# Performance work log

Measured on AMD Instinct MI355X. Metric: run time of the kernel, lower is better.

## Reference

```python
import jax, jax.numpy as jnp
import numpy as np
import math

B, S, E, H = 2, 8192, 1024, 16
D = E // H  # 64
CHUNK = 128


def _build_slopes(n):
    # ALiBi-style slopes (n is a power of 2 here)
    start = 2.0 ** (-(2.0 ** -(math.log2(n) - 3)))
    return np.array([start * (start ** i) for i in range(n)], dtype=np.float32)


def setup_inputs() -> dict:
    key = jax.random.key(0)
    ks = jax.random.split(key, 6)
    x = jax.random.normal(ks[0], (B, S, E), dtype=jnp.float32)
    # rotary table: (S, D//2, 2) = (cos, sin)
    inv_freq = 1.0 / (10000.0 ** (np.arange(0, D, 2, dtype=np.float32) / D))
    ang = np.arange(S, dtype=np.float32)[:, None] * inv_freq[None, :]  # (S, D/2)
    freqs_cis = jnp.asarray(np.stack([np.cos(ang), np.sin(ang)], axis=-1))
    wq = jax.random.normal(ks[1], (E, E), dtype=jnp.float32) * 0.02
    wk = jax.random.normal(ks[2], (E, E), dtype=jnp.float32) * 0.02
    wv = jax.random.normal(ks[3], (E, E), dtype=jnp.float32) * 0.02
    wo = jax.random.normal(ks[4], (E, E), dtype=jnp.float32) * 0.02
    rms_w = jnp.ones((E,), dtype=jnp.float32)
    return {"x": x, "freqs_cis": freqs_cis, "wq": wq, "wk": wk, "wv": wv, "wo": wo, "rms_w": rms_w}


def apply_rotary(x, fc):
    # x: (b, s, h, d); fc: (s, d/2, 2)
    xr = x.reshape(*x.shape[:-1], -1, 2)          # (b,s,h,d/2,2)
    fc = fc[None, :, None, :, :]                   # (1,s,1,d/2,2)
    out = jnp.stack([
        xr[..., 0] * fc[..., 0] - xr[..., 1] * fc[..., 1],
        xr[..., 1] * fc[..., 0] + xr[..., 0] * fc[..., 1],
    ], axis=-1)
    return out.reshape(x.shape)


def lightning_attn(q, k, v, slopes, C=CHUNK):
    # q,k,v: (B,H,S,D); per-head decay lambda = exp(-slope)
    Bs, Hs, Ss, Ds = q.shape
    NC = Ss // C
    j = jnp.arange(C, dtype=jnp.float32)
    diff = j[:, None] - j[None, :]
    s3 = slopes[:, None, None]                     # (H,1,1)
    Dmask = jnp.where(diff >= 0, jnp.exp(-s3 * diff), 0.0)   # (H,C,C) intra decay
    q_dec = jnp.exp(-slopes[:, None] * (j + 1.0))             # (H,C) cross-chunk q decay
    k_dec = jnp.exp(-slopes[:, None] * (C - 1.0 - j))         # (H,C) state-update k decay
    c_dec = jnp.exp(-slopes * C)[None, :, None, None]         # (1,H,1,1) full-chunk decay
    qc = q.reshape(Bs, Hs, NC, C, Ds).transpose(2, 0, 1, 3, 4)
    kc = k.reshape(Bs, Hs, NC, C, Ds).transpose(2, 0, 1, 3, 4)
    vc = v.reshape(Bs, Hs, NC, C, Ds).transpose(2, 0, 1, 3, 4)

    def step(St, inp):
        qb, kb, vb = inp                                       # (B,H,C,D)
        scores = jnp.einsum('bhid,bhjd->bhij', qb, kb) * Dmask[None]
        o = jnp.einsum('bhij,bhjd->bhid', scores, vb)
        o = o + q_dec[None, :, :, None] * jnp.einsum('bhid,bhde->bhie', qb, St)
        St = c_dec * St + jnp.einsum('bhcd,bhce->bhde', kb * k_dec[None, :, :, None], vb)
        return St, o

    S0 = jnp.zeros((Bs, Hs, Ds, Ds), dtype=jnp.float32)
    _, oc = jax.lax.scan(step, S0, (qc, kc, vc))               # oc: (NC,B,H,C,D)
    return oc.transpose(1, 2, 0, 3, 4).reshape(Bs, Hs, Ss, Ds)


def rms_norm(x, w, eps=1e-5):
    xf = x.astype(jnp.float32)
    n = xf * jax.lax.rsqrt(jnp.mean(xf * xf, axis=-1, keepdims=True) + eps)
    return n.astype(x.dtype) * w


def reference(x, freqs_cis, wq, wk, wv, wo, rms_w):
    b, s, _ = x.shape
    slopes = jnp.asarray(_build_slopes(H))
    q = (x @ wq.T).reshape(b, s, H, D)
    k = (x @ wk.T).reshape(b, s, H, D)
    v = (x @ wv.T).reshape(b, s, H, D)
    q = apply_rotary(q, freqs_cis)
    k = apply_rotary(k, freqs_cis)
    q = q.transpose(0, 2, 1, 3)   # (B,H,S,D)
    k = k.transpose(0, 2, 1, 3)
    v = v.transpose(0, 2, 1, 3)
    o = lightning_attn(q, k, v, slopes)             # (B,H,S,D)
    o = o.transpose(0, 2, 1, 3).reshape(b, s, E)    # b n (h d)
    o = rms_norm(o, rms_w)
    return o @ wo.T
```

## Files before the change

### kernel.cpp

```cpp
#include <hip/hip_runtime.h>


using h16   = _Float16;
using h16x8 = __attribute__((ext_vector_type(8))) _Float16;
using h16x4 = __attribute__((ext_vector_type(4))) _Float16;
using f32x4 = __attribute__((ext_vector_type(4))) float;

#define MFMA16(a,b,c) __builtin_amdgcn_mfma_f32_16x16x32_f16(a,b,c,0,0,0)

#define GLOAD16(gp, lp) __builtin_amdgcn_global_load_lds( \
    (const __attribute__((address_space(1))) void*)(gp),  \
    (__attribute__((address_space(3))) void*)(lp), 16, 0, 0)

__device__ __forceinline__ h16x8 rope8(h16x8 v, const float* __restrict__ fp) {
  float4 f0 = *(const float4*)fp;
  float4 f1 = *(const float4*)(fp + 4);
  h16x8 o; float x0, x1;
  x0=(float)v[0]; x1=(float)v[1]; o[0]=(h16)(x0*f0.x - x1*f0.y); o[1]=(h16)(x1*f0.x + x0*f0.y);
  x0=(float)v[2]; x1=(float)v[3]; o[2]=(h16)(x0*f0.z - x1*f0.w); o[3]=(h16)(x1*f0.z + x0*f0.w);
  x0=(float)v[4]; x1=(float)v[5]; o[4]=(h16)(x0*f1.x - x1*f1.y); o[5]=(h16)(x1*f1.x + x0*f1.y);
  x0=(float)v[6]; x1=(float)v[7]; o[6]=(h16)(x0*f1.z - x1*f1.w); o[7]=(h16)(x1*f1.z + x0*f1.w);
  return o;
}

__global__ __launch_bounds__(256) void k_cvt(const float* __restrict__ s,
                                             h16* __restrict__ d, int n) {
  int i = (blockIdx.x * 256 + threadIdx.x) * 8;
  if (i >= n) return;
  float4 a = *(const float4*)(s + i);
  float4 b = *(const float4*)(s + i + 4);
  h16x8 o;
  o[0]=(h16)a.x; o[1]=(h16)a.y; o[2]=(h16)a.z; o[3]=(h16)a.w;
  o[4]=(h16)b.x; o[5]=(h16)b.y; o[6]=(h16)b.z; o[7]=(h16)b.w;
  *(h16x8*)(d + i) = o;
}

__global__ __launch_bounds__(256) void k_cvt4(
    const float* __restrict__ s0, const float* __restrict__ s1,
    const float* __restrict__ s2, const float* __restrict__ s3,
    h16* __restrict__ d0, h16* __restrict__ d1,
    h16* __restrict__ d2, h16* __restrict__ d3) {
  const float* s = blockIdx.y == 0 ? s0 : (blockIdx.y == 1 ? s1 : (blockIdx.y == 2 ? s2 : s3));
  h16* d        = blockIdx.y == 0 ? d0 : (blockIdx.y == 1 ? d1 : (blockIdx.y == 2 ? d2 : d3));
  int i = (blockIdx.x * 256 + threadIdx.x) * 8;
  float4 a = *(const float4*)(s + i);
  float4 b = *(const float4*)(s + i + 4);
  h16x8 o;
  o[0]=(h16)a.x; o[1]=(h16)a.y; o[2]=(h16)a.z; o[3]=(h16)a.w;
  o[4]=(h16)b.x; o[5]=(h16)b.y; o[6]=(h16)b.z; o[7]=(h16)b.w;
  *(h16x8*)(d + i) = o;
}

__device__ __forceinline__ void gemm256_loop(
    const h16* __restrict__ At, const h16* __restrict__ Bt,
    char* smem, int w, int l, f32x4 (&acc)[8][4])
{
  const int tid = w*64 + l;
  const int wr = w >> 2, wc = w & 3;

  size_t gof[2];
  #pragma unroll
  for (int c = 0; c < 2; c++) {
    int G = c*512 + tid;
    int pp = G >> 3;
    int idx = (G & 7) ^ (pp & 7);
    gof[c] = (size_t)(2*pp + (idx >> 2))*1024 + (idx & 3)*8;
  }

  const int q16 = ((((l & 1) << 2) | (l >> 4)) ^ ((l >> 1) & 7)) * 16;
  const int abyte = wr*8192 + ((l >> 1) & 7)*128 + q16;
  const int bbyte = 16384 + wc*4096 + ((l >> 1) & 7)*128 + q16;

  auto stageA = [&](int kt) {
    char* buf = smem + (kt & 3)*32768;
    #pragma unroll
    for (int c = 0; c < 2; c++)
      GLOAD16(At + gof[c] + kt*32, buf + c*8192 + w*1024);
  };
  auto stageB = [&](int kt) {
    char* buf = smem + (kt & 3)*32768;
    #pragma unroll
    for (int c = 0; c < 2; c++)
      GLOAD16(Bt + gof[c] + kt*32, buf + 16384 + c*8192 + w*1024);
  };

  stageA(0); stageB(0); stageA(1); stageB(1);
  asm volatile("s_waitcnt vmcnt(4)" ::: "memory");
  __builtin_amdgcn_sched_barrier(0);
  __builtin_amdgcn_s_barrier();

  for (int t = 0; t < 32; ++t) {
    const char* buf = smem + (t & 3)*32768;
    h16x8 af[8], bf[4];
    #pragma unroll
    for (int mf = 0; mf < 4; mf++) af[mf] = *(const h16x8*)(buf + abyte + mf*1024);
    #pragma unroll
    for (int nf = 0; nf < 4; nf++) bf[nf] = *(const h16x8*)(buf + bbyte + nf*1024);
    if (t < 30) stageA(t + 2);
    asm volatile("s_waitcnt lgkmcnt(0)" ::: "memory");
    __builtin_amdgcn_sched_barrier(0);
    __builtin_amdgcn_s_setprio(1);
    #pragma unroll
    for (int mf = 0; mf < 4; mf++)
      #pragma unroll
      for (int nf = 0; nf < 4; nf++)
        acc[mf][nf] = MFMA16(af[mf], bf[nf], acc[mf][nf]);
    __builtin_amdgcn_s_setprio(0);
    #pragma unroll
    for (int mf = 0; mf < 4; mf++) af[4+mf] = *(const h16x8*)(buf + abyte + 4096 + mf*1024);
    if (t < 30) stageB(t + 2);
    asm volatile("s_waitcnt lgkmcnt(0)" ::: "memory");
    __builtin_amdgcn_sched_barrier(0);
    __builtin_amdgcn_s_setprio(1);
    #pragma unroll
    for (int mf = 0; mf < 4; mf++)
      #pragma unroll
      for (int nf = 0; nf < 4; nf++)
        acc[4+mf][nf] = MFMA16(af[4+mf], bf[nf], acc[4+mf][nf]);
    __builtin_amdgcn_s_setprio(0);
    if (t < 30)       asm volatile("s_waitcnt vmcnt(4)" ::: "memory");
    else if (t == 30) asm volatile("s_waitcnt vmcnt(0)" ::: "memory");
    if (t < 31) {
      __builtin_amdgcn_sched_barrier(0);
      __builtin_amdgcn_s_barrier();
    }
  }
}

__global__ __launch_bounds__(512, 2) void k_qkv(
    const h16* __restrict__ xh, const h16* __restrict__ w3,
    h16* __restrict__ qn, h16* __restrict__ kn, h16* __restrict__ vn)
{
  extern __shared__ __align__(16) char smem[];
  const int tid = threadIdx.x;
  const int w = tid >> 6, l = tid & 63;
  const int m0 = blockIdx.x * 256;
  const int nt = blockIdx.y;
  const int wr = w >> 2, wc = w & 3;

  f32x4 acc[8][4] = {};
  gemm256_loop(xh + (size_t)m0*1024, w3 + (size_t)(nt*256)*1024, smem, w, l, acc);

  const int proj = nt >> 2;
  h16* dst = proj == 0 ? qn : (proj == 1 ? kn : vn);
  const int cb = (nt & 3)*256 + wc*64;
  #pragma unroll
  for (int mf = 0; mf < 8; mf++)
    #pragma unroll
    for (int nf = 0; nf < 4; nf++)
      #pragma unroll
      for (int r = 0; r < 4; r++) {
        int row = wr*128 + mf*16 + ((l >> 4) << 2) + r;
        int col = cb + nf*16 + (l & 15);
        dst[(size_t)(m0 + row)*1024 + col] = (h16)acc[mf][nf][r];
      }
}

__global__ __launch_bounds__(512, 2) void k_out(
    const h16* __restrict__ an, const h16* __restrict__ woh,
    float* __restrict__ out)
{
  extern __shared__ __align__(16) char smem[];
  const int tid = threadIdx.x;
  const int w = tid >> 6, l = tid & 63;
  const int m0 = blockIdx.x * 256;
  const int n0 = blockIdx.y * 256;
  const int wr = w >> 2, wc = w & 3;

  f32x4 acc[8][4] = {};
  gemm256_loop(an + (size_t)m0*1024, woh + (size_t)n0*1024, smem, w, l, acc);

  #pragma unroll
  for (int mf = 0; mf < 8; mf++)
    #pragma unroll
    for (int nf = 0; nf < 4; nf++)
      #pragma unroll
      for (int r = 0; r < 4; r++) {
        int row = wr*128 + mf*16 + ((l >> 4) << 2) + r;
        int col = n0 + wc*64 + nf*16 + (l & 15);
        out[(size_t)(m0 + row)*1024 + col] = acc[mf][nf][r];
      }
}

__global__ __launch_bounds__(256) void k_trkv(
    const h16* __restrict__ kn, const h16* __restrict__ vn,
    const float* __restrict__ fc,
    h16* __restrict__ vt, h16* __restrict__ Th)
{
  __shared__ __align__(16) h16 tl[128*64];
  __shared__ __align__(16) h16 kT2[64*136];
  __shared__ __align__(16) h16 vT2[64*136];
  __shared__ float dt[128];
  const int tid = threadIdx.x;
  const int st = blockIdx.x;
  const int bh = blockIdx.y;
  const int b = bh >> 4, h = bh & 15;
  if (tid < 128) {
    float slope = exp2f(-0.5f * (float)(h + 1));
    dt[tid] = expf(-slope * (float)(127 - tid));
  }
  const size_t ibase = ((size_t)(b*8192 + st*128))*1024 + h*64;
  const size_t obase = (size_t)bh*64*8192 + st*128;
  const int cr = tid >> 3, c8 = tid & 7;

  for (int which = 0; which < 2; ++which) {
    const h16* src = which ? vn : kn;
    h16* dT2 = which ? vT2 : kT2;
    __syncthreads();
    #pragma unroll
    for (int i = 0; i < 4; i++) {
      int r = i*32 + cr;
      h16x8 v = *(const h16x8*)(src + ibase + (size_t)r*1024 + c8*8);
      if (!which) v = rope8(v, fc + (size_t)(st*128 + r)*64 + c8*8);
      int slot = (c8 + ((r >> 3) & 7)) & 7;
      *(h16x8*)(tl + r*64 + slot*8) = v;
    }
    __syncthreads();
    #pragma unroll
    for (int i = 0; i < 4; i++) {
      int chunk = i*256 + tid;
      int d = chunk >> 4;
      int j8 = chunk & 15;
      h16x8 o;
      #pragma unroll
      for (int jj = 0; jj < 8; jj++) {
        int c = j8*8 + jj;
        int pos = (d + ((c >> 3) & 7)*8) & 63;
        float fv = (float)tl[c*64 + pos];
        if (!which) fv *= dt[c];
        o[jj] = (h16)fv;
      }
      *(h16x8*)(dT2 + d*136 + j8*8) = o;
      if (which) *(h16x8*)(vt + obase + (size_t)d*8192 + j8*8) = o;
    }
  }
  __syncthreads();

  const int w = tid >> 6, l = tid & 63;
  f32x4 acc[4] = {};
  h16x8 a[4];
  #pragma unroll
  for (int ks = 0; ks < 4; ks++)
    a[ks] = *(const h16x8*)(vT2 + (w*16 + (l & 15))*136 + ks*32 + (l >> 4)*8);
  #pragma unroll
  for (int nf = 0; nf < 4; nf++) {
    #pragma unroll
    for (int ks = 0; ks < 4; ks++) {
      h16x8 bfr = *(const h16x8*)(kT2 + (nf*16 + (l & 15))*136 + ks*32 + (l >> 4)*8);
      acc[nf] = MFMA16(a[ks], bfr, acc[nf]);
    }
  }
  h16* Tb = Th + ((size_t)bh*64 + st)*4096;
  #pragma unroll
  for (int nf = 0; nf < 4; nf++)
    #pragma unroll
    for (int r = 0; r < 4; r++) {
      int e = w*16 + ((l >> 4) << 2) + r;
      int d = nf*16 + (l & 15);
      Tb[e*64 + d] = (h16)acc[nf][r];
    }
}

__global__ __launch_bounds__(256) void k_scan(const h16* __restrict__ Th,
                                              h16* __restrict__ ph) {
  const int bh = blockIdx.x;
  const int j  = blockIdx.y * 256 + threadIdx.x;
  const int h = bh & 15;
  const float cdec = expf(-exp2f(-0.5f*(float)(h+1)) * 128.0f);
  const h16* Tb = Th + (size_t)bh*64*4096 + j;
  h16* pb = ph + (size_t)bh*64*4096 + j;
  float run = 0.f;
  for (int t = 0; t < 64; t++) {
    float kv = (float)Tb[(size_t)t*4096];
    pb[(size_t)t*4096] = (h16)run;
    run = cdec*run + kv;
  }
}

__global__ __launch_bounds__(256) void k_att(
    const h16* __restrict__ qn, const h16* __restrict__ kn,
    const float* __restrict__ fc,
    const h16* __restrict__ vt, const h16* __restrict__ ph,
    h16* __restrict__ oh)
{
  __shared__ __align__(16) h16 P[128*144];
  __shared__ float dt[128], qd[128];
  const int tid = threadIdx.x;
  const int t = blockIdx.x;
  const int bh = blockIdx.y;
  const int b = bh >> 4, h = bh & 15;
  if (tid < 128) {
    float slope = exp2f(-0.5f*(float)(h+1));
    dt[tid] = expf(-slope*(float)tid);
    qd[tid] = expf(-slope*(float)(tid+1));
  }
  __syncthreads();
  const int w = tid >> 6, l = tid & 63;
  const int iw = w * 32;
  const h16* qb = qn + ((size_t)(b*8192 + t*128))*1024 + h*64;
  const h16* kb = kn + ((size_t)(b*8192 + t*128))*1024 + h*64;
  const h16* vb = vt + (size_t)bh*64*8192 + t*128;
  const h16* pb = ph + ((size_t)bh*64 + t)*4096;
  const float* fcb = fc + (size_t)(t*128)*64;

  h16x8 aq[2][2];
  #pragma unroll
  for (int mf = 0; mf < 2; mf++)
    #pragma unroll
    for (int ks = 0; ks < 2; ks++) {
      int row = iw + mf*16 + (l & 15);
      int d0 = ks*32 + (l >> 4)*8;
      aq[mf][ks] = rope8(*(const h16x8*)(qb + (size_t)row*1024 + d0),
                         fcb + (size_t)row*64 + d0);
    }

  f32x4 sc[2][8] = {};
  #pragma unroll
  for (int nf = 0; nf < 8; nf++) {
    if (nf*16 <= iw + 31) {
      #pragma unroll
      for (int ks = 0; ks < 2; ks++) {
        int row = nf*16 + (l & 15);
        int d0 = ks*32 + (l >> 4)*8;
        h16x8 bk = rope8(*(const h16x8*)(kb + (size_t)row*1024 + d0),
                         fcb + (size_t)row*64 + d0);
        sc[0][nf] = MFMA16(aq[0][ks], bk, sc[0][nf]);
        sc[1][nf] = MFMA16(aq[1][ks], bk, sc[1][nf]);
      }
    }
  }
  #pragma unroll
  for (int mf = 0; mf < 2; mf++) {
    #pragma unroll
    for (int nf = 0; nf < 8; nf++) {
      #pragma unroll
      for (int r = 0; r < 4; r++) {
        int i = iw + mf*16 + ((l >> 4) << 2) + r;
        int j = nf*16 + (l & 15);
        int diff = i - j;
        float v = diff >= 0 ? sc[mf][nf][r]*dt[diff] : 0.f;
        P[i*144 + j] = (h16)v;
      }
    }
  }
  f32x4 ao[2][4] = {};
  #pragma unroll
  for (int kc = 0; kc < 4; kc++) {
    h16x8 ap0 = *(const h16x8*)(P + (size_t)(iw + (l & 15))*144 + kc*32 + (l >> 4)*8);
    h16x8 ap1 = *(const h16x8*)(P + (size_t)(iw + 16 + (l & 15))*144 + kc*32 + (l >> 4)*8);
    #pragma unroll
    for (int nf = 0; nf < 4; nf++) {
      h16x8 bv = *(const h16x8*)(vb + (size_t)(nf*16 + (l & 15))*8192 + kc*32 + (l >> 4)*8);
      ao[0][nf] = MFMA16(ap0, bv, ao[0][nf]);
      ao[1][nf] = MFMA16(ap1, bv, ao[1][nf]);
    }
  }
  f32x4 a2[2][4] = {};
  #pragma unroll
  for (int ks = 0; ks < 2; ks++) {
    #pragma unroll
    for (int nf = 0; nf < 4; nf++) {
      h16x8 bs = *(const h16x8*)(pb + (size_t)(nf*16 + (l & 15))*64 + ks*32 + (l >> 4)*8);
      a2[0][nf] = MFMA16(aq[0][ks], bs, a2[0][nf]);
      a2[1][nf] = MFMA16(aq[1][ks], bs, a2[1][nf]);
    }
  }
  #pragma unroll
  for (int mf = 0; mf < 2; mf++) {
    #pragma unroll
    for (int nf = 0; nf < 4; nf++) {
      #pragma unroll
      for (int r = 0; r < 4; r++) {
        int i = iw + mf*16 + ((l >> 4) << 2) + r;
        int e = nf*16 + (l & 15);
        float o = ao[mf][nf][r] + qd[i]*a2[mf][nf][r];
        int s = t*128 + i;
        oh[((size_t)(b*8192 + s))*1024 + h*64 + e] = (h16)o;
      }
    }
  }
}

__global__ __launch_bounds__(256) void k_rms(const h16* __restrict__ o,
                                             const float* __restrict__ rw,
                                             h16* __restrict__ an) {
  const int tid = threadIdx.x;
  const size_t base = (size_t)blockIdx.x * 1024;
  h16x4 hv = *(const h16x4*)(o + base + tid*4);
  float v0 = (float)hv[0], v1 = (float)hv[1], v2 = (float)hv[2], v3 = (float)hv[3];
  float ss = v0*v0 + v1*v1 + v2*v2 + v3*v3;
  #pragma unroll
  for (int off = 32; off > 0; off >>= 1) ss += __shfl_down(ss, off);
  __shared__ float red[4];
  if ((tid & 63) == 0) red[tid >> 6] = ss;
  __syncthreads();
  float f = rsqrtf((red[0]+red[1]+red[2]+red[3]) * (1.0f/1024.0f) + 1e-5f);
  float4 wv = *(const float4*)(rw + tid*4);
  h16x4 r;
  r[0] = (h16)(v0*f*wv.x); r[1] = (h16)(v1*f*wv.y);
  r[2] = (h16)(v2*f*wv.z); r[3] = (h16)(v3*f*wv.w);
  *(h16x4*)(an + base + tid*4) = r;
}

extern "C" void kernel_launch(void* const* d_in, const int* in_sizes, int n_in,
                              void* d_out, int out_size, void* d_ws, size_t ws_size,
                              hipStream_t stream) {
  const float* x  = (const float*)d_in[0];
  const float* fc = (const float*)d_in[1];
  const float* wq = (const float*)d_in[2];
  const float* wk = (const float*)d_in[3];
  const float* wv = (const float*)d_in[4];
  const float* wo = (const float*)d_in[5];
  const float* rw = (const float*)d_in[6];
  float* out = (float*)d_out;

  char* p = (char*)d_ws;
  const size_t SZ = 33554432;
  h16* xh  = (h16*)(p);
  h16* vn  = (h16*)(p + 3*SZ);
  h16* Th  = (h16*)(p + 4*SZ);
  h16* vt  = (h16*)(p + 5*SZ);
  h16* oh  = (h16*)(p + 6*SZ);
  h16* w3  = (h16*)(p + 7*SZ);
  h16* woh = (h16*)(p + 7*SZ + 6291456);
  h16* qn = (h16*)out;
  h16* kn = (h16*)out + 16777216;

  (void)hipFuncSetAttribute((const void*)k_qkv, hipFuncAttributeMaxDynamicSharedMemorySize, 131072);
  (void)hipFuncSetAttribute((const void*)k_out, hipFuncAttributeMaxDynamicSharedMemorySize, 131072);

  hipLaunchKernelGGL(k_cvt, dim3(8192), dim3(256), 0, stream, x, xh, 16777216);
  hipLaunchKernelGGL(k_cvt4, dim3(512, 4), dim3(256), 0, stream,
                     wq, wk, wv, wo, w3, w3 + 1048576, w3 + 2097152, woh);

  hipLaunchKernelGGL(k_qkv, dim3(64, 12), dim3(512), 131072, stream, xh, w3, qn, kn, vn);
  hipLaunchKernelGGL(k_trkv, dim3(64, 32), dim3(256), 0, stream, kn, vn, fc, vt, Th);
  h16* ph = vn;
  hipLaunchKernelGGL(k_scan, dim3(32, 16), dim3(256), 0, stream, Th, ph);
  hipLaunchKernelGGL(k_att, dim3(64, 32), dim3(256), 0, stream, qn, kn, fc, vt, ph, oh);
  h16* an = xh;
  hipLaunchKernelGGL(k_rms, dim3(16384), dim3(256), 0, stream, oh, rw, an);
  hipLaunchKernelGGL(k_out, dim3(64, 4), dim3(512), 131072, stream, an, woh, out);
}
```

Measured before the change: 295.5 us.

## Fuse RMSNorm into output GEMM, store roped K, balance causal attention rows

Removes the separate RMSNorm kernel. The norm weight is folded into the converted wo weights, and each output block computes per-row inverse RMS scales, applied in the GEMM epilogue. The K/V transpose kernel now writes rotary-applied K in a head-contiguous layout, so the attention kernel no longer recomputes rope on K and reads contiguous rows. Attention warps now take a low and a mirrored high 16-row group, which balances the causal MFMA work across warps. The trade-offs are an extra K write, each out block re-reading its 256 rows to compute norms (done 4 times across the n-tiles), and a different fp16 rounding order.

```diff
diff --git a/kernel.cpp b/kernel.cpp
--- a/kernel.cpp
+++ b/kernel.cpp
@@ -38,6 +38,7 @@
 __global__ __launch_bounds__(256) void k_cvt4(
     const float* __restrict__ s0, const float* __restrict__ s1,
     const float* __restrict__ s2, const float* __restrict__ s3,
+    const float* __restrict__ rw,
     h16* __restrict__ d0, h16* __restrict__ d1,
     h16* __restrict__ d2, h16* __restrict__ d3) {
   const float* s = blockIdx.y == 0 ? s0 : (blockIdx.y == 1 ? s1 : (blockIdx.y == 2 ? s2 : s3));
@@ -45,6 +46,13 @@
   int i = (blockIdx.x * 256 + threadIdx.x) * 8;
   float4 a = *(const float4*)(s + i);
   float4 b = *(const float4*)(s + i + 4);
+  if (blockIdx.y == 3) {
+    const float* rp = rw + (i & 1023);
+    float4 r0 = *(const float4*)rp;
+    float4 r1 = *(const float4*)(rp + 4);
+    a.x*=r0.x; a.y*=r0.y; a.z*=r0.z; a.w*=r0.w;
+    b.x*=r1.x; b.y*=r1.y; b.z*=r1.z; b.w*=r1.w;
+  }
   h16x8 o;
   o[0]=(h16)a.x; o[1]=(h16)a.y; o[2]=(h16)a.z; o[3]=(h16)a.w;
   o[4]=(h16)b.x; o[5]=(h16)b.y; o[6]=(h16)b.z; o[7]=(h16)b.w;
@@ -157,18 +165,34 @@
 }
 
 __global__ __launch_bounds__(512, 2) void k_out(
-    const h16* __restrict__ an, const h16* __restrict__ woh,
+    const h16* __restrict__ oh, const h16* __restrict__ woh,
     float* __restrict__ out)
 {
   extern __shared__ __align__(16) char smem[];
+  __shared__ float pp[512];
+  __shared__ float rs[256];
   const int tid = threadIdx.x;
   const int w = tid >> 6, l = tid & 63;
   const int m0 = blockIdx.x * 256;
   const int n0 = blockIdx.y * 256;
   const int wr = w >> 2, wc = w & 3;
 
+  {
+    const int row = tid >> 1, half = tid & 1;
+    const h16* rp = oh + (size_t)(m0 + row)*1024 + half*512;
+    float ss = 0.f;
+    for (int i = 0; i < 64; i++) {
+      h16x8 v = *(const h16x8*)(rp + i*8);
+      #pragma unroll
+      for (int j = 0; j < 8; j++) { float f = (float)v[j]; ss += f*f; }
+    }
+    pp[tid] = ss;
+  }
+  __syncthreads();
+  if (tid < 256) rs[tid] = rsqrtf((pp[2*tid] + pp[2*tid+1])*(1.0f/1024.0f) + 1e-5f);
+
   f32x4 acc[8][4] = {};
-  gemm256_loop(an + (size_t)m0*1024, woh + (size_t)n0*1024, smem, w, l, acc);
+  gemm256_loop(oh + (size_t)m0*1024, woh + (size_t)n0*1024, smem, w, l, acc);
 
   #pragma unroll
   for (int mf = 0; mf < 8; mf++)
@@ -178,14 +202,14 @@
       for (int r = 0; r < 4; r++) {
         int row = wr*128 + mf*16 + ((l >> 4) << 2) + r;
         int col = n0 + wc*64 + nf*16 + (l & 15);
-        out[(size_t)(m0 + row)*1024 + col] = acc[mf][nf][r];
+        out[(size_t)(m0 + row)*1024 + col] = rs[row] * acc[mf][nf][r];
       }
 }
 
 __global__ __launch_bounds__(256) void k_trkv(
     const h16* __restrict__ kn, const h16* __restrict__ vn,
     const float* __restrict__ fc,
-    h16* __restrict__ vt, h16* __restrict__ Th)
+    h16* __restrict__ vt, h16* __restrict__ Th, h16* __restrict__ kr)
 {
   __shared__ __align__(16) h16 tl[128*64];
   __shared__ __align__(16) h16 kT2[64*136];
@@ -201,6 +225,7 @@
   }
   const size_t ibase = ((size_t)(b*8192 + st*128))*1024 + h*64;
   const size_t obase = (size_t)bh*64*8192 + st*128;
+  const size_t krbase = ((size_t)bh*8192 + st*128)*64;
   const int cr = tid >> 3, c8 = tid & 7;
 
   for (int which = 0; which < 2; ++which) {
@@ -211,7 +236,10 @@
     for (int i = 0; i < 4; i++) {
       int r = i*32 + cr;
       h16x8 v = *(const h16x8*)(src + ibase + (size_t)r*1024 + c8*8);
-      if (!which) v = rope8(v, fc + (size_t)(st*128 + r)*64 + c8*8);
+      if (!which) {
+        v = rope8(v, fc + (size_t)(st*128 + r)*64 + c8*8);
+        *(h16x8*)(kr + krbase + (size_t)r*64 + c8*8) = v;
+      }
       int slot = (c8 + ((r >> 3) & 7)) & 7;
       *(h16x8*)(tl + r*64 + slot*8) = v;
     }
@@ -278,7 +306,7 @@
 }
 
 __global__ __launch_bounds__(256) void k_att(
-    const h16* __restrict__ qn, const h16* __restrict__ kn,
+    const h16* __restrict__ qn, const h16* __restrict__ kr,
     const float* __restrict__ fc,
     const h16* __restrict__ vt, const h16* __restrict__ ph,
     h16* __restrict__ oh)
@@ -296,49 +324,48 @@
   }
   __syncthreads();
   const int w = tid >> 6, l = tid & 63;
-  const int iw = w * 32;
+  const int rb[2] = { w*16, (7 - w)*16 };
   const h16* qb = qn + ((size_t)(b*8192 + t*128))*1024 + h*64;
-  const h16* kb = kn + ((size_t)(b*8192 + t*128))*1024 + h*64;
+  const h16* kb = kr + ((size_t)bh*8192 + t*128)*64;
   const h16* vb = vt + (size_t)bh*64*8192 + t*128;
   const h16* pb = ph + ((size_t)bh*64 + t)*4096;
   const float* fcb = fc + (size_t)(t*128)*64;
 
   h16x8 aq[2][2];
   #pragma unroll
-  for (int mf = 0; mf < 2; mf++)
+  for (int g = 0; g < 2; g++)
     #pragma unroll
     for (int ks = 0; ks < 2; ks++) {
-      int row = iw + mf*16 + (l & 15);
+      int row = rb[g] + (l & 15);
       int d0 = ks*32 + (l >> 4)*8;
-      aq[mf][ks] = rope8(*(const h16x8*)(qb + (size_t)row*1024 + d0),
-                         fcb + (size_t)row*64 + d0);
+      aq[g][ks] = rope8(*(const h16x8*)(qb + (size_t)row*1024 + d0),
+                        fcb + (size_t)row*64 + d0);
     }
 
   f32x4 sc[2][8] = {};
   #pragma unroll
   for (int nf = 0; nf < 8; nf++) {
-    if (nf*16 <= iw + 31) {
+    const bool g0 = (nf <= w);
+    const bool g1 = (nf <= 7 - w);
+    if (g0 || g1) {
       #pragma unroll
       for (int ks = 0; ks < 2; ks++) {
-        int row = nf*16 + (l & 15);
-        int d0 = ks*32 + (l >> 4)*8;
-        h16x8 bk = rope8(*(const h16x8*)(kb + (size_t)row*1024 + d0),
-                         fcb + (size_t)row*64 + d0);
-        sc[0][nf] = MFMA16(aq[0][ks], bk, sc[0][nf]);
-        sc[1][nf] = MFMA16(aq[1][ks], bk, sc[1][nf]);
-      }
-    }
-  }
-  #pragma unroll
-  for (int mf = 0; mf < 2; mf++) {
+        h16x8 bk = *(const h16x8*)(kb + (size_t)(nf*16 + (l & 15))*64 + ks*32 + (l >> 4)*8);
+        if (g0) sc[0][nf] = MFMA16(aq[0][ks], bk, sc[0][nf]);
+        if (g1) sc[1][nf] = MFMA16(aq[1][ks], bk, sc[1][nf]);
+      }
+    }
+  }
+  #pragma unroll
+  for (int g = 0; g < 2; g++) {
     #pragma unroll
     for (int nf = 0; nf < 8; nf++) {
       #pragma unroll
       for (int r = 0; r < 4; r++) {
-        int i = iw + mf*16 + ((l >> 4) << 2) + r;
+        int i = rb[g] + ((l >> 4) << 2) + r;
         int j = nf*16 + (l & 15);
         int diff = i - j;
-        float v = diff >= 0 ? sc[mf][nf][r]*dt[diff] : 0.f;
+        float v = diff >= 0 ? sc[g][nf][r]*dt[diff] : 0.f;
         P[i*144 + j] = (h16)v;
       }
     }
@@ -346,8 +373,8 @@
   f32x4 ao[2][4] = {};
   #pragma unroll
   for (int kc = 0; kc < 4; kc++) {
-    h16x8 ap0 = *(const h16x8*)(P + (size_t)(iw + (l & 15))*144 + kc*32 + (l >> 4)*8);
-    h16x8 ap1 = *(const h16x8*)(P + (size_t)(iw + 16 + (l & 15))*144 + kc*32 + (l >> 4)*8);
+    h16x8 ap0 = *(const h16x8*)(P + (size_t)(rb[0] + (l & 15))*144 + kc*32 + (l >> 4)*8);
+    h16x8 ap1 = *(const h16x8*)(P + (size_t)(rb[1] + (l & 15))*144 + kc*32 + (l >> 4)*8);
     #pragma unroll
     for (int nf = 0; nf < 4; nf++) {
       h16x8 bv = *(const h16x8*)(vb + (size_t)(nf*16 + (l & 15))*8192 + kc*32 + (l >> 4)*8);
@@ -366,40 +393,19 @@
     }
   }
   #pragma unroll
-  for (int mf = 0; mf < 2; mf++) {
+  for (int g = 0; g < 2; g++) {
     #pragma unroll
     for (int nf = 0; nf < 4; nf++) {
       #pragma unroll
       for (int r = 0; r < 4; r++) {
-        int i = iw + mf*16 + ((l >> 4) << 2) + r;
+        int i = rb[g] + ((l >> 4) << 2) + r;
         int e = nf*16 + (l & 15);
-        float o = ao[mf][nf][r] + qd[i]*a2[mf][nf][r];
+        float o = ao[g][nf][r] + qd[i]*a2[g][nf][r];
         int s = t*128 + i;
         oh[((size_t)(b*8192 + s))*1024 + h*64 + e] = (h16)o;
       }
     }
   }
-}
-
-__global__ __launch_bounds__(256) void k_rms(const h16* __restrict__ o,
-                                             const float* __restrict__ rw,
-                                             h16* __restrict__ an) {
-  const int tid = threadIdx.x;
-  const size_t base = (size_t)blockIdx.x * 1024;
-  h16x4 hv = *(const h16x4*)(o + base + tid*4);
-  float v0 = (float)hv[0], v1 = (float)hv[1], v2 = (float)hv[2], v3 = (float)hv[3];
-  float ss = v0*v0 + v1*v1 + v2*v2 + v3*v3;
-  #pragma unroll
-  for (int off = 32; off > 0; off >>= 1) ss += __shfl_down(ss, off);
-  __shared__ float red[4];
-  if ((tid & 63) == 0) red[tid >> 6] = ss;
-  __syncthreads();
-  float f = rsqrtf((red[0]+red[1]+red[2]+red[3]) * (1.0f/1024.0f) + 1e-5f);
-  float4 wv = *(const float4*)(rw + tid*4);
-  h16x4 r;
-  r[0] = (h16)(v0*f*wv.x); r[1] = (h16)(v1*f*wv.y);
-  r[2] = (h16)(v2*f*wv.z); r[3] = (h16)(v3*f*wv.w);
-  *(h16x4*)(an + base + tid*4) = r;
 }
 
 extern "C" void kernel_launch(void* const* d_in, const int* in_sizes, int n_in,
@@ -431,14 +437,13 @@
 
   hipLaunchKernelGGL(k_cvt, dim3(8192), dim3(256), 0, stream, x, xh, 16777216);
   hipLaunchKernelGGL(k_cvt4, dim3(512, 4), dim3(256), 0, stream,
-                     wq, wk, wv, wo, w3, w3 + 1048576, w3 + 2097152, woh);
+                     wq, wk, wv, wo, rw, w3, w3 + 1048576, w3 + 2097152, woh);
 
   hipLaunchKernelGGL(k_qkv, dim3(64, 12), dim3(512), 131072, stream, xh, w3, qn, kn, vn);
-  hipLaunchKernelGGL(k_trkv, dim3(64, 32), dim3(256), 0, stream, kn, vn, fc, vt, Th);
+  h16* kr = xh;
+  hipLaunchKernelGGL(k_trkv, dim3(64, 32), dim3(256), 0, stream, kn, vn, fc, vt, Th, kr);
   h16* ph = vn;
   hipLaunchKernelGGL(k_scan, dim3(32, 16), dim3(256), 0, stream, Th, ph);
-  hipLaunchKernelGGL(k_att, dim3(64, 32), dim3(256), 0, stream, qn, kn, fc, vt, ph, oh);
-  h16* an = xh;
-  hipLaunchKernelGGL(k_rms, dim3(16384), dim3(256), 0, stream, oh, rw, an);
-  hipLaunchKernelGGL(k_out, dim3(64, 4), dim3(512), 131072, stream, an, woh, out);
-}
+  hipLaunchKernelGGL(k_att, dim3(64, 32), dim3(256), 0, stream, qn, kr, fc, vt, ph, oh);
+  hipLaunchKernelGGL(k_out, dim3(64, 4), dim3(512), 131072, stream, oh, woh, out);
+}
```

Result: no change. 293.6 us (-0.6%).
